# Kernel tuning notes

Measured on AMD Instinct MI355X. Metric: run time of the kernel, lower is better.

## Reference

```python
import jax, jax.numpy as jnp
import numpy as np

D_MODEL = 768
BOTTLENECK = 64
LN_EPS = 1e-5
SCALE = 1.0


def setup_inputs() -> dict:
    key = jax.random.key(0)
    k_x, k_wd = jax.random.split(key, 2)
    x = jax.random.normal(k_x, (8, 4096, D_MODEL), dtype=jnp.float32)
    # LayerNorm affine params
    ln_gamma = jnp.ones((D_MODEL,), dtype=jnp.float32)
    ln_beta = jnp.zeros((D_MODEL,), dtype=jnp.float32)
    # down_proj: kaiming_uniform_(a=sqrt(5)) -> bound = 1/sqrt(fan_in)
    bound = 1.0 / np.sqrt(D_MODEL)
    w_down = jax.random.uniform(k_wd, (D_MODEL, BOTTLENECK), dtype=jnp.float32,
                                minval=-bound, maxval=bound)
    b_down = jnp.zeros((BOTTLENECK,), dtype=jnp.float32)
    # up_proj initialized to zeros per 'lora' init; use small nonzero to make grads informative?
    # Stay faithful: zeros, as in the module's init.
    w_up = jnp.zeros((BOTTLENECK, D_MODEL), dtype=jnp.float32)
    b_up = jnp.zeros((D_MODEL,), dtype=jnp.float32)
    return {"x": x, "ln_gamma": ln_gamma, "ln_beta": ln_beta,
            "w_down": w_down, "b_down": b_down, "w_up": w_up, "b_up": b_up}


def _layer_norm(x, gamma, beta):
    mean = jnp.mean(x, axis=-1, keepdims=True)
    var = jnp.var(x, axis=-1, keepdims=True)
    return (x - mean) * jax.lax.rsqrt(var + LN_EPS) * gamma + beta


def reference(x, ln_gamma, ln_beta, w_down, b_down, w_up, b_up):
    # adapter_layernorm_option == 'in': LN before down projection
    h = _layer_norm(x, ln_gamma, ln_beta)              # [B, S, D]
    down = jnp.einsum('bsd,dk->bsk', h, w_down) + b_down  # [B, S, K]
    down = jax.nn.relu(down)
    # dropout is identity in eval mode
    out = jnp.einsum('bsk,kd->bsd', down, w_up) + b_up    # [B, S, D]
    return out * SCALE
```

## Files before the change

### kernel.cpp

```cpp
#include <hip/hip_runtime.h>
#include <hip/hip_bf16.h>


#define D_MODEL 768
#define KB      64
#define NTHR    256
#define PPAD    72

#define CH2     6
#define NCH2    8

typedef __attribute__((ext_vector_type(8))) short    bf16x8;
typedef __attribute__((ext_vector_type(4))) float    f32x4;
typedef __attribute__((ext_vector_type(4))) unsigned short us4;

static __device__ __forceinline__ unsigned short f2bf(float f) {
  unsigned int u = __builtin_bit_cast(unsigned int, f);
  unsigned int r = u + 0x7FFFu + ((u >> 16) & 1u);
  return (unsigned short)(r >> 16);
}

static __device__ __forceinline__ void gload16(const void* g, void* l) {
  __builtin_amdgcn_global_load_lds(
      (const __attribute__((address_space(1))) unsigned int*)g,
      (__attribute__((address_space(3))) unsigned int*)l, 16, 0, 0);
}

__global__ void __launch_bounds__(1024) adapter_prep(
    const float* __restrict__ wd,
    const float* __restrict__ wu,
    const float* __restrict__ gamma,
    const float* __restrict__ beta,
    const float* __restrict__ bdown,
    unsigned short* __restrict__ wdT,
    unsigned short* __restrict__ wuT,
    float* __restrict__ s_arr,
    float* __restrict__ t_arr) {
  const int b = blockIdx.x;
  const int t = threadIdx.x;
  if (b < 48) {
    const int i = b * 1024 + t;
    const int k1 = i / D_MODEL;
    const int d1 = i - k1 * D_MODEL;
    wdT[i] = f2bf(gamma[d1] * wd[(size_t)d1 * KB + k1]);
    const int d2 = i >> 6;
    const int k2 = i & 63;
    wuT[i] = f2bf(wu[(size_t)k2 * D_MODEL + d2]);
  } else {
    const int k = t & 63;
    const int c = t >> 6;
    float ss = 0.f, tt = 0.f;
    const int d0 = c * 48;
    #pragma unroll 4
    for (int d = d0; d < d0 + 48; ++d) {
      const float w = wd[(size_t)d * KB + k];
      ss = fmaf(gamma[d], w, ss);
      tt = fmaf(beta[d],  w, tt);
    }
    __shared__ float ps[16][64], pt[16][64];
    ps[c][k] = ss; pt[c][k] = tt;
    __syncthreads();
    if (t < 64) {
      float S = 0.f, T = 0.f;
      #pragma unroll
      for (int q = 0; q < 16; ++q) { S += ps[q][t]; T += pt[q][t]; }
      s_arr[t] = S;
      t_arr[t] = T + bdown[t];
    }
  }
}

__global__ void __launch_bounds__(NTHR, 2) adapter_main(
    const float* __restrict__ x,
    const float* __restrict__ s_arr,
    const float* __restrict__ t_arr,
    const unsigned short* __restrict__ wdT,
    const unsigned short* __restrict__ wuT,
    const float* __restrict__ b_up,
    float* __restrict__ out) {

  __shared__ __align__(16) unsigned char xs[4][2][8192];
  __shared__ unsigned short p_s[4][16][PPAD];

  const int t   = threadIdx.x;
  const int wid = t >> 6;
  const int l   = t & 63;
  const int lr  = l & 15;
  const int lg  = l >> 4;
  const int row0 = blockIdx.x * 64 + wid * 16;

  const float* xlane = x + (size_t)(row0 + lr) * D_MODEL + lg * 4;
  unsigned char* xb[2] = { &xs[wid][0][0], &xs[wid][1][0] };

  const unsigned short* wp = wdT + (size_t)lr * D_MODEL + 8 * lg;

  f32x4 acc[4];
  #pragma unroll
  for (int c = 0; c < 4; ++c) acc[c] = (f32x4){0.f, 0.f, 0.f, 0.f};
  float s1 = 0.f, s2 = 0.f;

  #pragma unroll
  for (int n = 0; n < 8; ++n)
    gload16(xlane + 32 * (n >> 1) + 16 * (n & 1), xb[0] + 1024 * n);

  #pragma unroll
  for (int ch = 0; ch < 6; ++ch) {
    const int cur = ch & 1;
    bf16x8 wf[4][4];
    #pragma unroll
    for (int c = 0; c < 4; ++c)
      #pragma unroll
      for (int j = 0; j < 4; ++j)
        wf[j][c] = *(const bf16x8*)(wp + (size_t)16 * c * D_MODEL + 32 * (4 * ch + j));
    if (ch < 5) {
      const float* g = xlane + 128 * (ch + 1);
      #pragma unroll
      for (int n = 0; n < 8; ++n)
        gload16(g + 32 * (n >> 1) + 16 * (n & 1), xb[cur ^ 1] + 1024 * n);
    }
    asm volatile("s_waitcnt vmcnt(0)" ::: "memory");
    __builtin_amdgcn_sched_barrier(0);
    #pragma unroll
    for (int j = 0; j < 4; ++j) {
      const unsigned char* cb = xb[cur] + 2048 * j + 512 * lg + 16 * lr;
      const f32x4 va = *(const f32x4*)(cb);
      const f32x4 vb = *(const f32x4*)(cb + 256);
      s1 += (va[0] + va[1]) + (va[2] + va[3]) + (vb[0] + vb[1]) + (vb[2] + vb[3]);
      s2 = fmaf(va[0], va[0], s2); s2 = fmaf(va[1], va[1], s2);
      s2 = fmaf(va[2], va[2], s2); s2 = fmaf(va[3], va[3], s2);
      s2 = fmaf(vb[0], vb[0], s2); s2 = fmaf(vb[1], vb[1], s2);
      s2 = fmaf(vb[2], vb[2], s2); s2 = fmaf(vb[3], vb[3], s2);
      bf16x8 xf;
      xf[0] = (short)f2bf(va[0]); xf[1] = (short)f2bf(va[1]);
      xf[2] = (short)f2bf(va[2]); xf[3] = (short)f2bf(va[3]);
      xf[4] = (short)f2bf(vb[0]); xf[5] = (short)f2bf(vb[1]);
      xf[6] = (short)f2bf(vb[2]); xf[7] = (short)f2bf(vb[3]);
      #pragma unroll
      for (int c = 0; c < 4; ++c)
        acc[c] = __builtin_amdgcn_mfma_f32_16x16x32_bf16(wf[j][c], xf, acc[c], 0, 0, 0);
    }
  }

  s1 += __shfl_xor(s1, 16); s1 += __shfl_xor(s1, 32);
  s2 += __shfl_xor(s2, 16); s2 += __shfl_xor(s2, 32);
  const float mu  = s1 * (1.0f / 768.0f);
  const float var = s2 * (1.0f / 768.0f) - mu * mu;
  const float rs  = rsqrtf(var + 1e-5f);
  const float nm  = -rs * mu;

  #pragma unroll
  for (int c = 0; c < 4; ++c) {
    const float4 sv = *(const float4*)(s_arr + 16 * c + 4 * lg);
    const float4 tv = *(const float4*)(t_arr + 16 * c + 4 * lg);
    us4 pk;
    pk.x = f2bf(fmaxf(fmaf(rs, acc[c][0], fmaf(nm, sv.x, tv.x)), 0.f));
    pk.y = f2bf(fmaxf(fmaf(rs, acc[c][1], fmaf(nm, sv.y, tv.y)), 0.f));
    pk.z = f2bf(fmaxf(fmaf(rs, acc[c][2], fmaf(nm, sv.z, tv.z)), 0.f));
    pk.w = f2bf(fmaxf(fmaf(rs, acc[c][3], fmaf(nm, sv.w, tv.w)), 0.f));
    *(us4*)&p_s[wid][lr][16 * c + 4 * lg] = pk;
  }

  const bf16x8 pa0 = *(const bf16x8*)&p_s[wid][lr][8 * lg];
  const bf16x8 pa1 = *(const bf16x8*)&p_s[wid][lr][32 + 8 * lg];
  float* op = out + (size_t)(row0 + 4 * lg) * D_MODEL + lr;

  bf16x8 wb[2][CH2][2];
  float  bb[2][CH2];
  #pragma unroll
  for (int j = 0; j < CH2; ++j) {
    const int cn = 16 * j;
    const unsigned short* bp = wuT + (size_t)(cn + lr) * KB + 8 * lg;
    wb[0][j][0] = *(const bf16x8*)(bp);
    wb[0][j][1] = *(const bf16x8*)(bp + 32);
    bb[0][j]    = b_up[cn + lr];
  }
  #pragma unroll
  for (int ch = 0; ch < NCH2; ++ch) {
    const int cur = ch & 1, nxt = cur ^ 1;
    if (ch < NCH2 - 1) {
      #pragma unroll
      for (int j = 0; j < CH2; ++j) {
        const int cn = 16 * (CH2 * (ch + 1) + j);
        const unsigned short* bp = wuT + (size_t)(cn + lr) * KB + 8 * lg;
        wb[nxt][j][0] = *(const bf16x8*)(bp);
        wb[nxt][j][1] = *(const bf16x8*)(bp + 32);
        bb[nxt][j]    = b_up[cn + lr];
      }
    }
    #pragma unroll
    for (int j = 0; j < CH2; ++j) {
      const int cn = 16 * (CH2 * ch + j);
      f32x4 c0 = {0.f, 0.f, 0.f, 0.f};
      c0 = __builtin_amdgcn_mfma_f32_16x16x32_bf16(pa0, wb[cur][j][0], c0, 0, 0, 0);
      c0 = __builtin_amdgcn_mfma_f32_16x16x32_bf16(pa1, wb[cur][j][1], c0, 0, 0, 0);
      const float bu = bb[cur][j];
      op[(size_t)0 * D_MODEL + cn] = c0[0] + bu;
      op[(size_t)1 * D_MODEL + cn] = c0[1] + bu;
      op[(size_t)2 * D_MODEL + cn] = c0[2] + bu;
      op[(size_t)3 * D_MODEL + cn] = c0[3] + bu;
    }
  }
}

extern "C" void kernel_launch(void* const* d_in, const int* in_sizes, int n_in,
                              void* d_out, int out_size, void* d_ws, size_t ws_size,
                              hipStream_t stream) {
  const float* x     = (const float*)d_in[0];
  const float* gamma = (const float*)d_in[1];
  const float* beta  = (const float*)d_in[2];
  const float* wd    = (const float*)d_in[3];
  const float* bdown = (const float*)d_in[4];
  const float* wu    = (const float*)d_in[5];
  const float* bup   = (const float*)d_in[6];
  float* out = (float*)d_out;

  char* ws = (char*)d_ws;
  unsigned short* wdT = (unsigned short*)ws;
  unsigned short* wuT = (unsigned short*)(ws + 98304);
  float* s_arr = (float*)(ws + 196608);
  float* t_arr = (float*)(ws + 196864);

  const int rows = in_sizes[0] / D_MODEL;

  adapter_prep<<<49, 1024, 0, stream>>>(wd, wu, gamma, beta, bdown,
                                        wdT, wuT, s_arr, t_arr);
  adapter_main<<<rows / 64, NTHR, 0, stream>>>(x, s_arr, t_arr, wdT, wuT, bup, out);
}
```

Before: 224.4 us.

## Restructure adapter kernel to 32-row blocks with shared x tile and LDS-staged output

```diff
diff --git a/kernel.cpp b/kernel.cpp
--- a/kernel.cpp
+++ b/kernel.cpp
@@ -4,15 +4,14 @@
 
 #define D_MODEL 768
 #define KB      64
+#define BMR     32
 #define NTHR    256
+#define XSTR    132
+#define OSTR    260
 #define PPAD    72
-
-#define CH2     6
-#define NCH2    8
 
 typedef __attribute__((ext_vector_type(8))) short    bf16x8;
 typedef __attribute__((ext_vector_type(4))) float    f32x4;
-typedef __attribute__((ext_vector_type(4))) unsigned short us4;
 
 static __device__ __forceinline__ unsigned short f2bf(float f) {
   unsigned int u = __builtin_bit_cast(unsigned int, f);
@@ -20,10 +19,19 @@
   return (unsigned short)(r >> 16);
 }
 
-static __device__ __forceinline__ void gload16(const void* g, void* l) {
+static __device__ __forceinline__ bf16x8 pack_bf8(const f32x4 a, const f32x4 b) {
+  union { __hip_bfloat162 h2[4]; bf16x8 v; } u;
+  u.h2[0] = __float22bfloat162_rn({a[0], a[1]});
+  u.h2[1] = __float22bfloat162_rn({a[2], a[3]});
+  u.h2[2] = __float22bfloat162_rn({b[0], b[1]});
+  u.h2[3] = __float22bfloat162_rn({b[2], b[3]});
+  return u.v;
+}
+
+static __device__ __forceinline__ void gload4(const float* g, float* lds) {
   __builtin_amdgcn_global_load_lds(
       (const __attribute__((address_space(1))) unsigned int*)g,
-      (__attribute__((address_space(3))) unsigned int*)l, 16, 0, 0);
+      (__attribute__((address_space(3))) unsigned int*)lds, 4, 0, 0);
 }
 
 __global__ void __launch_bounds__(1024) adapter_prep(
@@ -70,7 +78,7 @@
   }
 }
 
-__global__ void __launch_bounds__(NTHR, 2) adapter_main(
+__global__ void __launch_bounds__(NTHR, 4) adapter_main(
     const float* __restrict__ x,
     const float* __restrict__ s_arr,
     const float* __restrict__ t_arr,
@@ -79,125 +87,132 @@
     const float* __restrict__ b_up,
     float* __restrict__ out) {
 
-  __shared__ __align__(16) unsigned char xs[4][2][8192];
-  __shared__ unsigned short p_s[4][16][PPAD];
+  __shared__ __align__(16) unsigned char lds_raw[2 * BMR * XSTR * 4];
+  __shared__ unsigned short p_s[BMR][PPAD];
+
+  float* xs0 = (float*)lds_raw;
+  float* xs1 = (float*)(lds_raw + BMR * XSTR * 4);
+  float* os  = (float*)lds_raw;
 
   const int t   = threadIdx.x;
   const int wid = t >> 6;
   const int l   = t & 63;
   const int lr  = l & 15;
   const int lg  = l >> 4;
-  const int row0 = blockIdx.x * 64 + wid * 16;
-
-  const float* xlane = x + (size_t)(row0 + lr) * D_MODEL + lg * 4;
-  unsigned char* xb[2] = { &xs[wid][0][0], &xs[wid][1][0] };
-
-  const unsigned short* wp = wdT + (size_t)lr * D_MODEL + 8 * lg;
-
-  f32x4 acc[4];
-  #pragma unroll
-  for (int c = 0; c < 4; ++c) acc[c] = (f32x4){0.f, 0.f, 0.f, 0.f};
-  float s1 = 0.f, s2 = 0.f;
-
-  #pragma unroll
-  for (int n = 0; n < 8; ++n)
-    gload16(xlane + 32 * (n >> 1) + 16 * (n & 1), xb[0] + 1024 * n);
+  const int row0 = blockIdx.x * BMR;
+
+  auto stage = [&](int ck, float* buf) {
+    #pragma unroll
+    for (int i = 0; i < 8; ++i) {
+      const int r = 8 * wid + i;
+      const float* g0 = x + (size_t)(row0 + r) * D_MODEL + ck * 128 + l;
+      gload4(g0,      buf + r * XSTR);
+      gload4(g0 + 64, buf + r * XSTR + 64);
+    }
+  };
+
+  const unsigned short* wrow = wdT + (size_t)(16 * wid + lr) * D_MODEL + 8 * lg;
+
+  f32x4 acc0 = {0.f, 0.f, 0.f, 0.f};
+  f32x4 acc1 = {0.f, 0.f, 0.f, 0.f};
+  float s1a = 0.f, s2a = 0.f, s1b = 0.f, s2b = 0.f;
+
+  stage(0, xs0);
 
   #pragma unroll
   for (int ch = 0; ch < 6; ++ch) {
-    const int cur = ch & 1;
-    bf16x8 wf[4][4];
-    #pragma unroll
-    for (int c = 0; c < 4; ++c)
-      #pragma unroll
-      for (int j = 0; j < 4; ++j)
-        wf[j][c] = *(const bf16x8*)(wp + (size_t)16 * c * D_MODEL + 32 * (4 * ch + j));
-    if (ch < 5) {
-      const float* g = xlane + 128 * (ch + 1);
-      #pragma unroll
-      for (int n = 0; n < 8; ++n)
-        gload16(g + 32 * (n >> 1) + 16 * (n & 1), xb[cur ^ 1] + 1024 * n);
-    }
+    float* cb = (ch & 1) ? xs1 : xs0;
+    float* nb = (ch & 1) ? xs0 : xs1;
     asm volatile("s_waitcnt vmcnt(0)" ::: "memory");
     __builtin_amdgcn_sched_barrier(0);
-    #pragma unroll
-    for (int j = 0; j < 4; ++j) {
-      const unsigned char* cb = xb[cur] + 2048 * j + 512 * lg + 16 * lr;
-      const f32x4 va = *(const f32x4*)(cb);
-      const f32x4 vb = *(const f32x4*)(cb + 256);
-      s1 += (va[0] + va[1]) + (va[2] + va[3]) + (vb[0] + vb[1]) + (vb[2] + vb[3]);
-      s2 = fmaf(va[0], va[0], s2); s2 = fmaf(va[1], va[1], s2);
-      s2 = fmaf(va[2], va[2], s2); s2 = fmaf(va[3], va[3], s2);
-      s2 = fmaf(vb[0], vb[0], s2); s2 = fmaf(vb[1], vb[1], s2);
-      s2 = fmaf(vb[2], vb[2], s2); s2 = fmaf(vb[3], vb[3], s2);
-      bf16x8 xf;
-      xf[0] = (short)f2bf(va[0]); xf[1] = (short)f2bf(va[1]);
-      xf[2] = (short)f2bf(va[2]); xf[3] = (short)f2bf(va[3]);
-      xf[4] = (short)f2bf(vb[0]); xf[5] = (short)f2bf(vb[1]);
-      xf[6] = (short)f2bf(vb[2]); xf[7] = (short)f2bf(vb[3]);
+    __syncthreads();
+    if (ch < 5) stage(ch + 1, nb);
+    #pragma unroll
+    for (int kkL = 0; kkL < 4; ++kkL) {
+      const int kk = 4 * ch + kkL;
+      const bf16x8 wq = *(const bf16x8*)(wrow + 32 * kk);
+      const float* pa_ = cb + lr * XSTR + kkL * 32 + 8 * lg;
+      const float* pb_ = cb + (16 + lr) * XSTR + kkL * 32 + 8 * lg;
+      const f32x4 a0 = *(const f32x4*)(pa_);
+      const f32x4 a1 = *(const f32x4*)(pa_ + 4);
+      const f32x4 b0 = *(const f32x4*)(pb_);
+      const f32x4 b1 = *(const f32x4*)(pb_ + 4);
+      s1a += (a0[0] + a0[1]) + (a0[2] + a0[3]) + (a1[0] + a1[1]) + (a1[2] + a1[3]);
+      s2a = fmaf(a0[0], a0[0], s2a); s2a = fmaf(a0[1], a0[1], s2a);
+      s2a = fmaf(a0[2], a0[2], s2a); s2a = fmaf(a0[3], a0[3], s2a);
+      s2a = fmaf(a1[0], a1[0], s2a); s2a = fmaf(a1[1], a1[1], s2a);
+      s2a = fmaf(a1[2], a1[2], s2a); s2a = fmaf(a1[3], a1[3], s2a);
+      s1b += (b0[0] + b0[1]) + (b0[2] + b0[3]) + (b1[0] + b1[1]) + (b1[2] + b1[3]);
+      s2b = fmaf(b0[0], b0[0], s2b); s2b = fmaf(b0[1], b0[1], s2b);
+      s2b = fmaf(b0[2], b0[2], s2b); s2b = fmaf(b0[3], b0[3], s2b);
+      s2b = fmaf(b1[0], b1[0], s2b); s2b = fmaf(b1[1], b1[1], s2b);
+      s2b = fmaf(b1[2], b1[2], s2b); s2b = fmaf(b1[3], b1[3], s2b);
+      const bf16x8 xa = pack_bf8(a0, a1);
+      const bf16x8 xb = pack_bf8(b0, b1);
+      acc0 = __builtin_amdgcn_mfma_f32_16x16x32_bf16(xa, wq, acc0, 0, 0, 0);
+      acc1 = __builtin_amdgcn_mfma_f32_16x16x32_bf16(xb, wq, acc1, 0, 0, 0);
+    }
+  }
+
+  s1a += __shfl_xor(s1a, 16); s1a += __shfl_xor(s1a, 32);
+  s2a += __shfl_xor(s2a, 16); s2a += __shfl_xor(s2a, 32);
+  s1b += __shfl_xor(s1b, 16); s1b += __shfl_xor(s1b, 32);
+  s2b += __shfl_xor(s2b, 16); s2b += __shfl_xor(s2b, 32);
+
+  const int pcol = 16 * wid + lr;
+  const float sk = s_arr[pcol];
+  const float tk = t_arr[pcol];
+  #pragma unroll
+  for (int j = 0; j < 4; ++j) {
+    const float ma1 = __shfl(s1a, 4 * lg + j), ma2 = __shfl(s2a, 4 * lg + j);
+    const float mb1 = __shfl(s1b, 4 * lg + j), mb2 = __shfl(s2b, 4 * lg + j);
+    const float mua = ma1 * (1.0f / 768.0f);
+    const float rsa = rsqrtf(ma2 * (1.0f / 768.0f) - mua * mua + 1e-5f);
+    const float mub = mb1 * (1.0f / 768.0f);
+    const float rsb = rsqrtf(mb2 * (1.0f / 768.0f) - mub * mub + 1e-5f);
+    const float da = fmaxf(fmaf(rsa, acc0[j], fmaf(-rsa * mua, sk, tk)), 0.f);
+    const float db = fmaxf(fmaf(rsb, acc1[j], fmaf(-rsb * mub, sk, tk)), 0.f);
+    p_s[4 * lg + j][pcol]      = f2bf(da);
+    p_s[16 + 4 * lg + j][pcol] = f2bf(db);
+  }
+
+  __syncthreads();
+
+  bf16x8 pA[2][2];
+  pA[0][0] = *(const bf16x8*)&p_s[lr][8 * lg];
+  pA[0][1] = *(const bf16x8*)&p_s[lr][32 + 8 * lg];
+  pA[1][0] = *(const bf16x8*)&p_s[16 + lr][8 * lg];
+  pA[1][1] = *(const bf16x8*)&p_s[16 + lr][32 + 8 * lg];
+
+  #pragma unroll
+  for (int g = 0; g < 3; ++g) {
+    if (g) __syncthreads();
+    #pragma unroll
+    for (int q = 0; q < 4; ++q) {
+      const int col = 256 * g + 64 * wid + 16 * q + lr;
+      const unsigned short* bp = wuT + (size_t)col * KB + 8 * lg;
+      const bf16x8 wb0 = *(const bf16x8*)(bp);
+      const bf16x8 wb1 = *(const bf16x8*)(bp + 32);
+      f32x4 c0 = {0.f, 0.f, 0.f, 0.f};
+      f32x4 c1 = {0.f, 0.f, 0.f, 0.f};
+      c0 = __builtin_amdgcn_mfma_f32_16x16x32_bf16(pA[0][0], wb0, c0, 0, 0, 0);
+      c0 = __builtin_amdgcn_mfma_f32_16x16x32_bf16(pA[0][1], wb1, c0, 0, 0, 0);
+      c1 = __builtin_amdgcn_mfma_f32_16x16x32_bf16(pA[1][0], wb0, c1, 0, 0, 0);
+      c1 = __builtin_amdgcn_mfma_f32_16x16x32_bf16(pA[1][1], wb1, c1, 0, 0, 0);
+      const float bu = b_up[col];
+      const int cl = 64 * wid + 16 * q + lr;
       #pragma unroll
-      for (int c = 0; c < 4; ++c)
-        acc[c] = __builtin_amdgcn_mfma_f32_16x16x32_bf16(wf[j][c], xf, acc[c], 0, 0, 0);
-    }
-  }
-
-  s1 += __shfl_xor(s1, 16); s1 += __shfl_xor(s1, 32);
-  s2 += __shfl_xor(s2, 16); s2 += __shfl_xor(s2, 32);
-  const float mu  = s1 * (1.0f / 768.0f);
-  const float var = s2 * (1.0f / 768.0f) - mu * mu;
-  const float rs  = rsqrtf(var + 1e-5f);
-  const float nm  = -rs * mu;
-
-  #pragma unroll
-  for (int c = 0; c < 4; ++c) {
-    const float4 sv = *(const float4*)(s_arr + 16 * c + 4 * lg);
-    const float4 tv = *(const float4*)(t_arr + 16 * c + 4 * lg);
-    us4 pk;
-    pk.x = f2bf(fmaxf(fmaf(rs, acc[c][0], fmaf(nm, sv.x, tv.x)), 0.f));
-    pk.y = f2bf(fmaxf(fmaf(rs, acc[c][1], fmaf(nm, sv.y, tv.y)), 0.f));
-    pk.z = f2bf(fmaxf(fmaf(rs, acc[c][2], fmaf(nm, sv.z, tv.z)), 0.f));
-    pk.w = f2bf(fmaxf(fmaf(rs, acc[c][3], fmaf(nm, sv.w, tv.w)), 0.f));
-    *(us4*)&p_s[wid][lr][16 * c + 4 * lg] = pk;
-  }
-
-  const bf16x8 pa0 = *(const bf16x8*)&p_s[wid][lr][8 * lg];
-  const bf16x8 pa1 = *(const bf16x8*)&p_s[wid][lr][32 + 8 * lg];
-  float* op = out + (size_t)(row0 + 4 * lg) * D_MODEL + lr;
-
-  bf16x8 wb[2][CH2][2];
-  float  bb[2][CH2];
-  #pragma unroll
-  for (int j = 0; j < CH2; ++j) {
-    const int cn = 16 * j;
-    const unsigned short* bp = wuT + (size_t)(cn + lr) * KB + 8 * lg;
-    wb[0][j][0] = *(const bf16x8*)(bp);
-    wb[0][j][1] = *(const bf16x8*)(bp + 32);
-    bb[0][j]    = b_up[cn + lr];
-  }
-  #pragma unroll
-  for (int ch = 0; ch < NCH2; ++ch) {
-    const int cur = ch & 1, nxt = cur ^ 1;
-    if (ch < NCH2 - 1) {
-      #pragma unroll
-      for (int j = 0; j < CH2; ++j) {
-        const int cn = 16 * (CH2 * (ch + 1) + j);
-        const unsigned short* bp = wuT + (size_t)(cn + lr) * KB + 8 * lg;
-        wb[nxt][j][0] = *(const bf16x8*)(bp);
-        wb[nxt][j][1] = *(const bf16x8*)(bp + 32);
-        bb[nxt][j]    = b_up[cn + lr];
+      for (int j = 0; j < 4; ++j) {
+        os[(4 * lg + j) * OSTR + cl]        = c0[j] + bu;
+        os[(16 + 4 * lg + j) * OSTR + cl]   = c1[j] + bu;
       }
     }
-    #pragma unroll
-    for (int j = 0; j < CH2; ++j) {
-      const int cn = 16 * (CH2 * ch + j);
-      f32x4 c0 = {0.f, 0.f, 0.f, 0.f};
-      c0 = __builtin_amdgcn_mfma_f32_16x16x32_bf16(pa0, wb[cur][j][0], c0, 0, 0, 0);
-      c0 = __builtin_amdgcn_mfma_f32_16x16x32_bf16(pa1, wb[cur][j][1], c0, 0, 0, 0);
-      const float bu = bb[cur][j];
-      op[(size_t)0 * D_MODEL + cn] = c0[0] + bu;
-      op[(size_t)1 * D_MODEL + cn] = c0[1] + bu;
-      op[(size_t)2 * D_MODEL + cn] = c0[2] + bu;
-      op[(size_t)3 * D_MODEL + cn] = c0[3] + bu;
+    __syncthreads();
+    #pragma unroll
+    for (int i = 0; i < 8; ++i) {
+      const int r = 8 * wid + i;
+      const f32x4 v = *(const f32x4*)&os[r * OSTR + 4 * l];
+      *(f32x4*)(out + (size_t)(row0 + r) * D_MODEL + 256 * g + 4 * l) = v;
     }
   }
 }
@@ -224,5 +239,5 @@
 
   adapter_prep<<<49, 1024, 0, stream>>>(wd, wu, gamma, beta, bdown,
                                         wdT, wuT, s_arr, t_arr);
-  adapter_main<<<rows / 64, NTHR, 0, stream>>>(x, s_arr, t_arr, wdT, wuT, bup, out);
-}
+  adapter_main<<<rows / BMR, NTHR, 0, stream>>>(x, s_arr, t_arr, wdT, wuT, bup, out);
+}
```

Result: faster. 203.3 us (-9.4%).
